# Kernel optimization log

Measured on AMD Instinct MI355X. Metric: run time of the kernel, lower is better.

The kernel has to match this reference:

```python
import jax, jax.numpy as jnp
import numpy as np

S = 7
BATCH = 8192
LAMBDA_COORD = 5.0
LAMBDA_NOOBJ = 0.5
EPS = 1e-06


def setup_inputs() -> dict:
    key = jax.random.key(0)
    k1, k2, k3 = jax.random.split(key, 3)
    predicts = jax.random.uniform(k1, (BATCH, S, S, 30), dtype=jnp.float32)
    targets = jax.random.uniform(k2, (BATCH, S, S, 30), dtype=jnp.float32)
    keep = jax.random.uniform(k3, (BATCH, S, S)) < 0.25
    conf = jnp.where(keep, targets[..., 4], 0.0)
    targets = targets.at[..., 4].set(conf).at[..., 9].set(conf)
    return {"predicts": predicts, "targets": targets}


def _cxcywh_to_xyxy(cx, cy, w, h):
    return cx - w / 2, cy - h / 2, cx + w / 2, cy + h / 2


def _elementwise_iou(a, b):
    # a, b: tuples (cx, cy, w, h) of [batch, S, S] arrays.
    # Equivalent to torchvision box_iou(A, B).diag() but computed per-cell (no N^2 matrix).
    ax1, ay1, ax2, ay2 = _cxcywh_to_xyxy(*a)
    bx1, by1, bx2, by2 = _cxcywh_to_xyxy(*b)
    iw = jnp.clip(jnp.minimum(ax2, bx2) - jnp.maximum(ax1, bx1), 0.0)
    ih = jnp.clip(jnp.minimum(ay2, by2) - jnp.maximum(ay1, by1), 0.0)
    inter = iw * ih
    area_a = (ax2 - ax1) * (ay2 - ay1)
    area_b = (bx2 - bx1) * (by2 - by1)
    return inter / (area_a + area_b - inter)


def reference(predicts, targets):
    pre1 = predicts[..., :5]
    pre2 = predicts[..., 5:10]
    pre_cls = predicts[..., 10:]
    tar = targets[..., :5]
    tar_cls = targets[..., 10:]

    obj = targets[..., 4] > 0  # [B, S, S]
    noobj = ~obj

    gx = jnp.arange(S, dtype=predicts.dtype)[None, :]  # grid_x, broadcast over rows
    gy = jnp.arange(S, dtype=predicts.dtype)[:, None]  # grid_y, broadcast over cols
    ratio = 1.0 / S

    def to_abs(b):
        return ((b[..., 0] + gx) * ratio, (b[..., 1] + gy) * ratio, b[..., 2], b[..., 3])

    abs1, abs2, abst = to_abs(pre1), to_abs(pre2), to_abs(tar)
    iou1 = _elementwise_iou(abs1, abst)  # [B, S, S]
    iou2 = _elementwise_iou(abs2, abst)
    resp = iou1 > iou2

    m1 = (obj & resp).astype(predicts.dtype)   # box1 responsible
    m2 = (obj & ~resp).astype(predicts.dtype)  # box2 responsible
    mo = obj.astype(predicts.dtype)
    mn = noobj.astype(predicts.dtype)

    # coordinate losses (sum-reduced masked MSE)
    loss_xy = jnp.sum(m1[..., None] * (pre1[..., :2] - tar[..., :2]) ** 2) + \
              jnp.sum(m2[..., None] * (pre2[..., :2] - tar[..., :2]) ** 2)
    sq = lambda x: jnp.sqrt(jnp.clip(x, EPS))
    loss_wh = jnp.sum(m1[..., None] * (sq(pre1[..., 2:4]) - sq(tar[..., 2:4])) ** 2) + \
              jnp.sum(m2[..., None] * (sq(pre2[..., 2:4]) - sq(tar[..., 2:4])) ** 2)
    coord_loss = LAMBDA_COORD * (loss_xy + loss_wh)

    # confidence losses (note: IoU target is NOT detached in the original)
    conf_obj = jnp.sum(m1 * (pre1[..., 4] - iou1) ** 2) + \
               jnp.sum(m2 * (pre2[..., 4] - iou2) ** 2)
    conf_noobj = LAMBDA_NOOBJ * (jnp.sum(mn * pre1[..., 4] ** 2) +
                                 jnp.sum(mn * pre2[..., 4] ** 2))

    # class loss
    cls_loss = jnp.sum(mo[..., None] * (pre_cls - tar_cls) ** 2)

    return coord_loss + conf_obj + conf_noobj + cls_loss
```

## Files before the change

kernel.cpp:

```cpp
#include <hip/hip_runtime.h>
#include <math.h>


#define S7 7
#define CCH 30
#define CELLS_PER_BLOCK 256
#define N_CELLS (8192 * S7 * S7)
#define N_BLOCKS (N_CELLS / CELLS_PER_BLOCK)
#define EPSV 1e-6f

__device__ __forceinline__ float iou_cxcywh(float acx, float acy, float aw, float ah,
                                            float bcx, float bcy, float bw, float bh) {
    float ax1 = acx - aw * 0.5f, ax2 = acx + aw * 0.5f;
    float ay1 = acy - ah * 0.5f, ay2 = acy + ah * 0.5f;
    float bx1 = bcx - bw * 0.5f, bx2 = bcx + bw * 0.5f;
    float by1 = bcy - bh * 0.5f, by2 = bcy + bh * 0.5f;
    float iw = fmaxf(fminf(ax2, bx2) - fmaxf(ax1, bx1), 0.0f);
    float ih = fmaxf(fminf(ay2, by2) - fmaxf(ay1, by1), 0.0f);
    float inter = iw * ih;
    float area_a = (ax2 - ax1) * (ay2 - ay1);
    float area_b = (bx2 - bx1) * (by2 - by1);
    return inter / (area_a + area_b - inter);
}

__global__ __launch_bounds__(256) void yolo_loss_partial(const float* __restrict__ pred,
                                                         const float* __restrict__ targ,
                                                         float* __restrict__ partial) {
    __shared__ float sp[CELLS_PER_BLOCK * CCH];
    __shared__ float st[CELLS_PER_BLOCK * CCH];

    const int tid = threadIdx.x;
    const int block_cell0 = blockIdx.x * CELLS_PER_BLOCK;

    const float4* p4 = (const float4*)(pred + (size_t)block_cell0 * CCH);
    const float4* t4 = (const float4*)(targ + (size_t)block_cell0 * CCH);
    float4* sp4 = (float4*)sp;
    float4* st4 = (float4*)st;
#pragma unroll
    for (int k = tid; k < 1920; k += 256) {
        sp4[k] = p4[k];
        st4[k] = t4[k];
    }
    __syncthreads();

    const float* p = sp + tid * CCH;
    const float* t = st + tid * CCH;
    const int cell = block_cell0 + tid;
    const int xy = cell % (S7 * S7);
    const float fx = (float)(xy % S7);
    const float fy = (float)(xy / S7);
    const float ratio = 1.0f / 7.0f;

    float px1 = p[0], py1 = p[1], pw1 = p[2], ph1 = p[3], pc1 = p[4];
    float px2 = p[5], py2 = p[6], pw2 = p[7], ph2 = p[8], pc2 = p[9];
    float tx = t[0], ty = t[1], tw = t[2], th = t[3], tc = t[4];
    bool obj = tc > 0.0f;

    float tcx = (tx + fx) * ratio, tcy = (ty + fy) * ratio;
    float iou1 = iou_cxcywh((px1 + fx) * ratio, (py1 + fy) * ratio, pw1, ph1,
                            tcx, tcy, tw, th);
    float iou2 = iou_cxcywh((px2 + fx) * ratio, (py2 + fy) * ratio, pw2, ph2,
                            tcx, tcy, tw, th);
    bool resp = iou1 > iou2;

    float cls = 0.0f;
#pragma unroll
    for (int k = 10; k < 30; ++k) {
        float d = p[k] - t[k];
        cls += d * d;
    }

    float loss;
    if (obj) {
        float sx, sy, sw, sh, sc, siou;
        if (resp) { sx = px1; sy = py1; sw = pw1; sh = ph1; sc = pc1; siou = iou1; }
        else      { sx = px2; sy = py2; sw = pw2; sh = ph2; sc = pc2; siou = iou2; }
        float dx = sx - tx, dy = sy - ty;
        float dw = sqrtf(fmaxf(sw, EPSV)) - sqrtf(fmaxf(tw, EPSV));
        float dh = sqrtf(fmaxf(sh, EPSV)) - sqrtf(fmaxf(th, EPSV));
        float dc = sc - siou;
        loss = 5.0f * (dx * dx + dy * dy + dw * dw + dh * dh) + dc * dc + cls;
    } else {
        loss = 0.5f * (pc1 * pc1 + pc2 * pc2);
    }

    float v = loss;
#pragma unroll
    for (int off = 32; off > 0; off >>= 1) v += __shfl_down(v, off);

    __shared__ float red[4];
    const int lane = tid & 63;
    const int wid = tid >> 6;
    if (lane == 0) red[wid] = v;
    __syncthreads();
    if (tid == 0) partial[blockIdx.x] = red[0] + red[1] + red[2] + red[3];
}

__global__ __launch_bounds__(256) void yolo_loss_final(const float* __restrict__ partial,
                                                       float* __restrict__ out) {
    float v = 0.0f;
    for (int i = threadIdx.x; i < N_BLOCKS; i += 256) v += partial[i];
#pragma unroll
    for (int off = 32; off > 0; off >>= 1) v += __shfl_down(v, off);

    __shared__ float red[4];
    const int lane = threadIdx.x & 63;
    const int wid = threadIdx.x >> 6;
    if (lane == 0) red[wid] = v;
    __syncthreads();
    if (threadIdx.x == 0) out[0] = red[0] + red[1] + red[2] + red[3];
}

extern "C" void kernel_launch(void* const* d_in, const int* in_sizes, int n_in,
                              void* d_out, int out_size, void* d_ws, size_t ws_size,
                              hipStream_t stream) {
    const float* predicts = (const float*)d_in[0];
    const float* targets  = (const float*)d_in[1];
    float* out = (float*)d_out;
    float* partial = (float*)d_ws;

    yolo_loss_partial<<<N_BLOCKS, 256, 0, stream>>>(predicts, targets, partial);
    yolo_loss_final<<<1, 256, 0, stream>>>(partial, out);
}
```

Measured before the change: 120.5 us.

## Fuse final reduction into main kernel via last-block atomic counter

Folds the separate final-reduction kernel into the main kernel: each block publishes its partial sum with a release store, bumps an atomic counter, and the last block to finish sums all partials and writes the result. The load loop is also restructured to issue all global float4 loads into registers before writing them to shared memory, so more memory requests are in flight at once. This removes one kernel launch and its dependency gap but adds a memset call, atomic traffic, and extra register pressure.

```diff
diff --git a/kernel.cpp b/kernel.cpp
--- a/kernel.cpp
+++ b/kernel.cpp
@@ -23,24 +23,31 @@
     return inter / (area_a + area_b - inter);
 }
 
-__global__ __launch_bounds__(256) void yolo_loss_partial(const float* __restrict__ pred,
-                                                         const float* __restrict__ targ,
-                                                         float* __restrict__ partial) {
+__global__ __launch_bounds__(256) void yolo_loss_fused(const float* __restrict__ pred,
+                                                       const float* __restrict__ targ,
+                                                       float* __restrict__ out,
+                                                       unsigned int* __restrict__ counter,
+                                                       float* __restrict__ partial) {
     __shared__ float sp[CELLS_PER_BLOCK * CCH];
     __shared__ float st[CELLS_PER_BLOCK * CCH];
 
     const int tid = threadIdx.x;
-    const int block_cell0 = blockIdx.x * CELLS_PER_BLOCK;
+    const int bid = blockIdx.x;
+    const int block_cell0 = bid * CELLS_PER_BLOCK;
 
     const float4* p4 = (const float4*)(pred + (size_t)block_cell0 * CCH);
     const float4* t4 = (const float4*)(targ + (size_t)block_cell0 * CCH);
     float4* sp4 = (float4*)sp;
     float4* st4 = (float4*)st;
+
+    float4 rp[8], rt[8];
 #pragma unroll
-    for (int k = tid; k < 1920; k += 256) {
-        sp4[k] = p4[k];
-        st4[k] = t4[k];
-    }
+    for (int j = 0; j < 7; ++j) { rp[j] = p4[tid + 256 * j]; rt[j] = t4[tid + 256 * j]; }
+    const bool extra = tid < 128;
+    if (extra) { rp[7] = p4[tid + 1792]; rt[7] = t4[tid + 1792]; }
+#pragma unroll
+    for (int j = 0; j < 7; ++j) { sp4[tid + 256 * j] = rp[j]; st4[tid + 256 * j] = rt[j]; }
+    if (extra) { sp4[tid + 1792] = rp[7]; st4[tid + 1792] = rt[7]; }
     __syncthreads();
 
     const float* p = sp + tid * CCH;
@@ -89,26 +96,31 @@
     for (int off = 32; off > 0; off >>= 1) v += __shfl_down(v, off);
 
     __shared__ float red[4];
+    __shared__ bool is_last;
     const int lane = tid & 63;
     const int wid = tid >> 6;
     if (lane == 0) red[wid] = v;
     __syncthreads();
-    if (tid == 0) partial[blockIdx.x] = red[0] + red[1] + red[2] + red[3];
-}
 
-__global__ __launch_bounds__(256) void yolo_loss_final(const float* __restrict__ partial,
-                                                       float* __restrict__ out) {
-    float v = 0.0f;
-    for (int i = threadIdx.x; i < N_BLOCKS; i += 256) v += partial[i];
+    if (tid == 0) {
+        float bsum = red[0] + red[1] + red[2] + red[3];
+        __hip_atomic_store(&partial[bid], bsum, __ATOMIC_RELEASE, __HIP_MEMORY_SCOPE_AGENT);
+        unsigned int prev = __hip_atomic_fetch_add(counter, 1u, __ATOMIC_ACQ_REL,
+                                                   __HIP_MEMORY_SCOPE_AGENT);
+        is_last = (prev == (unsigned int)(N_BLOCKS - 1));
+    }
+    __syncthreads();
+
+    if (is_last) {
+        float s = 0.0f;
+        for (int i = tid; i < N_BLOCKS; i += 256)
+            s += __hip_atomic_load(&partial[i], __ATOMIC_RELAXED, __HIP_MEMORY_SCOPE_AGENT);
 #pragma unroll
-    for (int off = 32; off > 0; off >>= 1) v += __shfl_down(v, off);
-
-    __shared__ float red[4];
-    const int lane = threadIdx.x & 63;
-    const int wid = threadIdx.x >> 6;
-    if (lane == 0) red[wid] = v;
-    __syncthreads();
-    if (threadIdx.x == 0) out[0] = red[0] + red[1] + red[2] + red[3];
+        for (int off = 32; off > 0; off >>= 1) s += __shfl_down(s, off);
+        if (lane == 0) red[wid] = s;
+        __syncthreads();
+        if (tid == 0) out[0] = red[0] + red[1] + red[2] + red[3];
+    }
 }
 
 extern "C" void kernel_launch(void* const* d_in, const int* in_sizes, int n_in,
@@ -117,8 +129,11 @@
     const float* predicts = (const float*)d_in[0];
     const float* targets  = (const float*)d_in[1];
     float* out = (float*)d_out;
-    float* partial = (float*)d_ws;
 
-    yolo_loss_partial<<<N_BLOCKS, 256, 0, stream>>>(predicts, targets, partial);
-    yolo_loss_final<<<1, 256, 0, stream>>>(partial, out);
+    unsigned int* counter = (unsigned int*)d_ws;
+    float* partial = (float*)((char*)d_ws + 256);
+
+    hipMemsetAsync(counter, 0, sizeof(unsigned int), stream);
+
+    yolo_loss_fused<<<N_BLOCKS, 256, 0, stream>>>(predicts, targets, out, counter, partial);
 }
```

Measured after the change: 262.8 us. 2.18x slower.
